# Performance work log

Hardware: AMD Instinct MI355X
Metric: run time of the kernel (lower is better)

## Reference

```python
import jax, jax.numpy as jnp
import numpy as np

B = 16384
SEQ_DIM = 512
EPI_DIM = 512
IN_DIM = SEQ_DIM + EPI_DIM   # 1024
OUT_DIM = 1024
N_EXPERTS = 8
LN_EPS = 1e-5


def setup_inputs() -> dict:
    key = jax.random.key(0)
    ks = jax.random.split(key, 10)
    s_in = 1.0 / np.sqrt(IN_DIM)
    s_out = 1.0 / np.sqrt(OUT_DIM)
    return {
        "z_s": jax.random.normal(ks[0], (B, SEQ_DIM), dtype=jnp.float32),
        "z_e": jax.random.normal(ks[1], (B, EPI_DIM), dtype=jnp.float32),
        # router: Linear(IN_DIM, N_EXPERTS)
        "router_w": jax.random.uniform(ks[2], (IN_DIM, N_EXPERTS), jnp.float32, -s_in, s_in),
        "router_b": jax.random.uniform(ks[3], (N_EXPERTS,), jnp.float32, -s_in, s_in),
        # expert layer 1: Linear(IN_DIM, OUT_DIM), stacked over experts
        "w1": jax.random.uniform(ks[4], (N_EXPERTS, IN_DIM, OUT_DIM), jnp.float32, -s_in, s_in),
        "b1": jax.random.uniform(ks[5], (N_EXPERTS, OUT_DIM), jnp.float32, -s_in, s_in),
        # expert layer 2: Linear(OUT_DIM, OUT_DIM)
        "w2": jax.random.uniform(ks[6], (N_EXPERTS, OUT_DIM, OUT_DIM), jnp.float32, -s_out, s_out),
        "b2": jax.random.uniform(ks[7], (N_EXPERTS, OUT_DIM), jnp.float32, -s_out, s_out),
        # per-expert LayerNorm affine params
        "gamma": jnp.ones((N_EXPERTS, OUT_DIM), dtype=jnp.float32),
        "beta": jnp.zeros((N_EXPERTS, OUT_DIM), dtype=jnp.float32),
    }


def reference(z_s, z_e, router_w, router_b, w1, b1, w2, b2, gamma, beta):
    combined = jnp.concatenate([z_s, z_e], axis=-1)            # [B, IN_DIM]
    weights = jax.nn.softmax(combined @ router_w + router_b, axis=-1)  # [B, E]
    # all experts as one batched GEMM (dropout = identity in eval mode)
    h = jnp.einsum('bi,eih->beh', combined, w1) + b1           # [B, E, H]
    h = jax.nn.gelu(h, approximate=False)
    y = jnp.einsum('beh,eho->beo', h, w2) + b2                 # [B, E, H]
    # per-expert LayerNorm over last dim
    mu = jnp.mean(y, axis=-1, keepdims=True)
    var = jnp.mean(jnp.square(y - mu), axis=-1, keepdims=True)
    y = (y - mu) * jax.lax.rsqrt(var + LN_EPS) * gamma + beta
    # softmax-weighted sum over experts
    z = jnp.einsum('be,beo->bo', weights, y)                   # [B, H]
    return z
```

## Files before the change

### kernel.cpp

```cpp
#include <hip/hip_runtime.h>
#include <cstdint>
#include <cstddef>

#define NEXP 8

typedef __attribute__((ext_vector_type(8))) short short8;
typedef __attribute__((ext_vector_type(4))) float f32x4;

static __device__ __forceinline__ float bf2f(unsigned short u) {
  union { unsigned int i; float f; } v; v.i = ((unsigned int)u) << 16; return v.f;
}
static __device__ __forceinline__ unsigned short f2bf(float f) {
  union { float f; unsigned int i; } v; v.f = f;
  unsigned int x = v.i;
  return (unsigned short)((x + 0x7fffu + ((x >> 16) & 1u)) >> 16);
}

static __device__ __forceinline__ float gelu_fast(float x) {
  const float u = 0.7978845608028654f * (x + 0.044715f * x * x * x);
  const float t = 1.0f - 2.0f / (__expf(2.0f * u) + 1.0f);
  return 0.5f * x * (1.0f + t);
}

__device__ __forceinline__ void gload16(const void* g, void* l) {
  __builtin_amdgcn_global_load_lds(
      (const __attribute__((address_space(1))) void*)g,
      (__attribute__((address_space(3))) void*)l, 16, 0, 0);
}

#define BAR() __builtin_amdgcn_s_barrier()
#define WAIT_LGKM0() asm volatile("s_waitcnt lgkmcnt(0)" ::: "memory")

__global__ __launch_bounds__(256) void prep_kernel(
    const float* __restrict__ z_s, const float* __restrict__ z_e,
    const float* __restrict__ rw, const float* __restrict__ rb,
    const float* __restrict__ w1, const float* __restrict__ w2,
    unsigned short* __restrict__ Xb, float* __restrict__ wts,
    unsigned short* __restrict__ wt1, unsigned short* __restrict__ wt2)
{
  __shared__ float red[4][NEXP];
  __shared__ unsigned short tile[32][33];
  const int bid = blockIdx.x;
  const int t = threadIdx.x;

  if (bid < 16384) {
    const int b = bid;
    const float* src = (t < 128) ? (z_s + (size_t)b * 512 + t * 4)
                                 : (z_e + (size_t)b * 512 + (t - 128) * 4);
    float4 v = *(const float4*)src;

    ushort4 o;
    o.x = f2bf(v.x); o.y = f2bf(v.y); o.z = f2bf(v.z); o.w = f2bf(v.w);
    *(ushort4*)(Xb + (size_t)b * 1024 + t * 4) = o;

    float acc[NEXP];
#pragma unroll
    for (int e = 0; e < NEXP; ++e) acc[e] = 0.f;

    const int k0 = t * 4;
    const float xv[4] = { v.x, v.y, v.z, v.w };
#pragma unroll
    for (int j = 0; j < 4; ++j) {
      const float x = xv[j];
      const float4* rwp = (const float4*)(rw + (size_t)(k0 + j) * NEXP);
      float4 r0 = rwp[0], r1 = rwp[1];
      acc[0] += x * r0.x; acc[1] += x * r0.y; acc[2] += x * r0.z; acc[3] += x * r0.w;
      acc[4] += x * r1.x; acc[5] += x * r1.y; acc[6] += x * r1.z; acc[7] += x * r1.w;
    }

#pragma unroll
    for (int off = 32; off; off >>= 1) {
#pragma unroll
      for (int e = 0; e < NEXP; ++e) acc[e] += __shfl_xor(acc[e], off);
    }
    if ((t & 63) == 0) {
#pragma unroll
      for (int e = 0; e < NEXP; ++e) red[t >> 6][e] = acc[e];
    }
    __syncthreads();
    if (t == 0) {
      float lg[NEXP];
      float mx = -1e30f;
#pragma unroll
      for (int e = 0; e < NEXP; ++e) {
        lg[e] = red[0][e] + red[1][e] + red[2][e] + red[3][e] + rb[e];
        mx = fmaxf(mx, lg[e]);
      }
      float sum = 0.f;
#pragma unroll
      for (int e = 0; e < NEXP; ++e) { lg[e] = expf(lg[e] - mx); sum += lg[e]; }
      const float inv = 1.f / sum;
#pragma unroll
      for (int e = 0; e < NEXP; ++e) wts[(size_t)b * NEXP + e] = lg[e] * inv;
    }
  } else {
    const int z = (bid - 16384) >> 10;
    const int r = (bid - 16384) & 1023;
    const int k0 = (r >> 5) * 32, n0 = (r & 31) * 32;
    const float* w = (z < 8) ? w1 : w2;
    unsigned short* wt = (z < 8) ? wt1 : wt2;
    const int e = z & 7;
    const int tx = t & 31, ty = t >> 5;

    const float* wp = w + ((size_t)e << 20) + (size_t)k0 * 1024 + n0;
#pragma unroll
    for (int i = 0; i < 4; ++i) {
      const int kk = ty + i * 8;
      tile[kk][tx] = f2bf(wp[(size_t)kk * 1024 + tx]);
    }
    __syncthreads();
    unsigned short* op = wt + ((size_t)e << 20) + (size_t)n0 * 1024 + k0;
#pragma unroll
    for (int i = 0; i < 4; ++i) {
      const int nn = ty + i * 8;
      op[(size_t)nn * 1024 + tx] = tile[tx][nn];
    }
  }
}

template <bool GELU>
__global__ __launch_bounds__(512, 2) void gemm8_kernel(
    const unsigned short* __restrict__ A,
    const unsigned short* __restrict__ Bt,
    const float* __restrict__ bias,
    unsigned short* __restrict__ C,
    long long strideAe, long long strideCe, int mtiles)
{
  __shared__ unsigned short lds[65536];

  const int nwg = gridDim.x;
  const int cpx = nwg >> 3;
  const int bid = blockIdx.x;
  const int swz = (bid & 7) * cpx + (bid >> 3);
  const int e   = swz / (mtiles << 2);
  const int rem = swz - e * (mtiles << 2);
  const int m0  = (rem >> 2) << 8;
  const int n0  = (rem & 3) << 8;

  const int t   = threadIdx.x;
  const int l   = t & 63;
  const int wid = t >> 6;
  const int wm  = wid >> 2;
  const int wn  = wid & 3;

  const unsigned short* Ae = A + (size_t)e * strideAe + (size_t)m0 * 1024;
  const unsigned short* Be = Bt + ((size_t)e << 20) + (size_t)n0 * 1024;

  const int sr = t >> 3;
  const int ss = ((t & 7) ^ ((t >> 3) & 7)) * 8;

  auto stageA = [&](int d, int h, int T) {
    const unsigned short* g = Ae + (size_t)(h * 128 + sr) * 1024 + T * 64 + ss;
    unsigned short* lp = lds + d * 32768 + h * 8192 + t * 8;
    gload16(g, lp);
    gload16(g + 65536, lp + 4096);
  };
  auto stageB = [&](int d, int h, int T) {
    const unsigned short* g = Be + (size_t)(h * 128 + sr) * 1024 + T * 64 + ss;
    unsigned short* lp = lds + 16384 + d * 32768 + h * 8192 + t * 8;
    gload16(g, lp);
    gload16(g + 65536, lp + 4096);
  };

  const int kq  = (l >> 4) ^ (l & 3);
  const int b2p = (l >> 2) & 1;
  const int sl0 = ((b2p << 2) | kq) * 8;
  const int sl1 = (((b2p ^ 1) << 2) | kq) * 8;
  const int aR = wm * 8192 + (l & 15) * 64;
  const int bR = 16384 + (wn >> 1) * 8192 + (wn & 1) * 4096 + (l & 15) * 64;

  short8 a[4][2], b0[2][2], b1[2][2];
  f32x4 acc[8][4];
#pragma unroll
  for (int i = 0; i < 8; ++i)
#pragma unroll
    for (int j = 0; j < 4; ++j) acc[i][j] = (f32x4){0.f, 0.f, 0.f, 0.f};

  auto ldA = [&](int d, int q) {
#pragma unroll
    for (int m = 0; m < 4; ++m) {
      const unsigned short* p = lds + d * 32768 + aR + (q * 4 + m) * 1024;
      a[m][0] = *(const short8*)(p + sl0);
      a[m][1] = *(const short8*)(p + sl1);
    }
  };
  auto ldB = [&](int d, int q, short8 (&br)[2][2]) {
#pragma unroll
    for (int n = 0; n < 2; ++n) {
      const unsigned short* p = lds + d * 32768 + bR + (q * 2 + n) * 1024;
      br[n][0] = *(const short8*)(p + sl0);
      br[n][1] = *(const short8*)(p + sl1);
    }
  };
  auto mmac = [&](int aq, int bq, short8 (&br)[2][2]) {
    __builtin_amdgcn_s_setprio(1);
#pragma unroll
    for (int ks = 0; ks < 2; ++ks)
#pragma unroll
      for (int m = 0; m < 4; ++m)
#pragma unroll
        for (int n = 0; n < 2; ++n)
          acc[aq * 4 + m][bq * 2 + n] = __builtin_amdgcn_mfma_f32_16x16x32_bf16(
              a[m][ks], br[n][ks], acc[aq * 4 + m][bq * 2 + n], 0, 0, 0);
    __builtin_amdgcn_s_setprio(0);
  };

  stageA(0, 0, 0); stageA(0, 1, 0); stageB(0, 0, 0); stageB(0, 1, 0);
  stageB(1, 0, 1); stageB(1, 1, 1); stageA(1, 0, 1);
  asm volatile("s_waitcnt vmcnt(6)" ::: "memory");
  BAR();

#pragma unroll 1
  for (int i = 0; i < 8; ++i) {
    const bool nl = (i < 7);
    const int T1 = 2 * i + 1, T2 = 2 * i + 2, T3 = 2 * i + 3;
    ldA(0, 0); ldB(0, 0, b0); stageA(1, 1, T1);
    asm volatile("s_waitcnt lgkmcnt(8)" ::: "memory");
    BAR(); WAIT_LGKM0();
    mmac(0, 0, b0);
    BAR();
    ldB(0, 1, b1);
    BAR(); WAIT_LGKM0();
    mmac(0, 1, b1);
    BAR();
    ldA(0, 1);
    if (nl) stageB(0, 0, T2);
    BAR(); WAIT_LGKM0();
    mmac(1, 1, b1);
    BAR();
    if (nl) { stageB(0, 1, T2); stageA(0, 0, T2); }
    BAR();
    mmac(1, 0, b0);
    if (nl) asm volatile("s_waitcnt vmcnt(6)" ::: "memory");
    else    asm volatile("s_waitcnt vmcnt(0)" ::: "memory");
    BAR();
    ldA(1, 0); ldB(1, 0, b0);
    if (nl) stageA(0, 1, T2);
    asm volatile("s_waitcnt lgkmcnt(8)" ::: "memory");
    BAR(); WAIT_LGKM0();
    mmac(0, 0, b0);
    BAR();
    ldB(1, 1, b1);
    BAR(); WAIT_LGKM0();
    mmac(0, 1, b1);
    BAR();
    ldA(1, 1);
    if (nl) stageB(1, 0, T3);
    BAR(); WAIT_LGKM0();
    mmac(1, 1, b1);
    BAR();
    if (nl) { stageB(1, 1, T3); stageA(1, 0, T3); }
    BAR();
    mmac(1, 0, b0);
    if (nl) asm volatile("s_waitcnt vmcnt(6)" ::: "memory");
    BAR();
  }

  const float* bp = bias + (size_t)e * 1024 + n0 + wn * 64;
  unsigned short* Ce = C + (size_t)e * strideCe + (size_t)(m0 + wm * 128) * 1024 + n0 + wn * 64;
  const int cr = (l >> 4) * 4, cc = l & 15;
#pragma unroll
  for (int mi = 0; mi < 8; ++mi) {
#pragma unroll
    for (int ni = 0; ni < 4; ++ni) {
      const int col = ni * 16 + cc;
      const float bv = bp[col];
#pragma unroll
      for (int r = 0; r < 4; ++r) {
        float v = acc[mi][ni][r] + bv;
        if (GELU) v = gelu_fast(v);
        Ce[(size_t)(mi * 16 + cr + r) * 1024 + col] = f2bf(v);
      }
    }
  }
}

__global__ __launch_bounds__(512) void finalize_kernel(
    const unsigned short* __restrict__ y,
    const float* __restrict__ wts,
    const float* __restrict__ gamma,
    const float* __restrict__ beta,
    float* __restrict__ zout,
    int Bc, int bbase)
{
  __shared__ float zacc[NEXP][1024];
  const int brow = blockIdx.x;
  const int t = threadIdx.x;
  const int e = t >> 6;
  const int lane = t & 63;

  const unsigned short* yp = y + ((size_t)e * Bc + brow) * 1024;
  short8 v0 = *(const short8*)(yp + lane * 8);
  short8 v1 = *(const short8*)(yp + 512 + lane * 8);

  float f0[8], f1[8];
  float s = 0.f, sq = 0.f;
#pragma unroll
  for (int j = 0; j < 8; ++j) {
    f0[j] = bf2f((unsigned short)v0[j]);
    f1[j] = bf2f((unsigned short)v1[j]);
    s += f0[j] + f1[j];
    sq += f0[j] * f0[j] + f1[j] * f1[j];
  }
#pragma unroll
  for (int off = 32; off; off >>= 1) {
    s  += __shfl_xor(s, off);
    sq += __shfl_xor(sq, off);
  }
  const float mu  = s * (1.f / 1024.f);
  const float var = sq * (1.f / 1024.f) - mu * mu;
  const float rs  = rsqrtf(var + 1e-5f);
  const float w   = wts[(size_t)(bbase + brow) * NEXP + e];

  const int c0 = lane * 8;
#pragma unroll
  for (int j = 0; j < 8; ++j) {
    const int ca = c0 + j, cb = 512 + c0 + j;
    zacc[e][ca] = w * ((f0[j] - mu) * rs * gamma[e * 1024 + ca] + beta[e * 1024 + ca]);
    zacc[e][cb] = w * ((f1[j] - mu) * rs * gamma[e * 1024 + cb] + beta[e * 1024 + cb]);
  }
  __syncthreads();
  float r0 = 0.f, r1 = 0.f;
#pragma unroll
  for (int ee = 0; ee < NEXP; ++ee) { r0 += zacc[ee][t]; r1 += zacc[ee][t + 512]; }
  float* zp = zout + (size_t)(bbase + brow) * 1024;
  zp[t] = r0;
  zp[t + 512] = r1;
}

extern "C" void kernel_launch(void* const* d_in, const int* in_sizes, int n_in,
                              void* d_out, int out_size, void* d_ws, size_t ws_size,
                              hipStream_t stream)
{
  const float* z_s      = (const float*)d_in[0];
  const float* z_e      = (const float*)d_in[1];
  const float* router_w = (const float*)d_in[2];
  const float* router_b = (const float*)d_in[3];
  const float* w1       = (const float*)d_in[4];
  const float* b1       = (const float*)d_in[5];
  const float* w2       = (const float*)d_in[6];
  const float* b2       = (const float*)d_in[7];
  const float* gamma    = (const float*)d_in[8];
  const float* beta     = (const float*)d_in[9];
  float* zout = (float*)d_out;

  const int B = 16384;

  char* ws = (char*)d_ws;
  unsigned short* Xb  = (unsigned short*)ws;
  unsigned short* W1t = (unsigned short*)(ws + 33554432);
  unsigned short* W2t = W1t + ((size_t)8 << 20);
  float* wts = (float*)(ws + 33554432 + 2 * 16777216);
  const size_t persist = 33554432 + 2 * 16777216 + 524288;
  char* dyn = ws + persist;
  const size_t rem = (ws_size > persist) ? (ws_size - persist) : 0;

  int nch = 2;
  while ((size_t)(B / nch) * 32768ull > rem && nch < 64) nch <<= 1;
  const int Bc = B / nch;

  unsigned short* hbuf = (unsigned short*)dyn;
  unsigned short* ybuf = hbuf + (size_t)Bc * 8 * 1024;

  prep_kernel<<<32768, 256, 0, stream>>>(z_s, z_e, router_w, router_b, w1, w2,
                                         Xb, wts, W1t, W2t);

  const int mt = Bc >> 8;
  const int nwg = mt * 32;

  for (int c = 0; c < nch; ++c) {
    const int bbase = c * Bc;
    gemm8_kernel<true><<<nwg, 512, 0, stream>>>(
        Xb + (size_t)bbase * 1024, W1t, b1, hbuf, 0ll, (long long)Bc * 1024, mt);
    gemm8_kernel<false><<<nwg, 512, 0, stream>>>(
        hbuf, W2t, b2, ybuf, (long long)Bc * 1024, (long long)Bc * 1024, mt);
    finalize_kernel<<<Bc, 512, 0, stream>>>(ybuf, wts, gamma, beta, zout, Bc, bbase);
  }
}
```

Before: 762.0 us.

## Fuse prep, both GEMMs and finalize into one persistent kernel with grid barriers

Replaces the prep kernel and the per-chunk GEMM1/GEMM2/finalize launches with a single persistent kernel of 256 workgroups. Phases are separated by atomic-counter grid barriers, and GEMM tiles and finalize rows are statically assigned per workgroup. The aim is to remove launch gaps and per-kernel tail effects between the many dependent stages. In exchange it adds spin-barrier overhead, relies on all 256 workgroups being co-resident to avoid deadlock, and runs the conversion/transpose prep with far fewer workgroups than before.

```diff
diff --git a/kernel.cpp b/kernel.cpp
--- a/kernel.cpp
+++ b/kernel.cpp
@@ -3,6 +3,7 @@
 #include <cstddef>
 
 #define NEXP 8
+#define NBLK 256
 
 typedef __attribute__((ext_vector_type(8))) short short8;
 typedef __attribute__((ext_vector_type(4))) float f32x4;
@@ -23,7 +24,8 @@
 }
 
 __device__ __forceinline__ void gload16(const void* g, void* l) {
-  __builtin_amdgcn_global_load_lds(
+  __builtin_amdgcn_global_lo\
+ad_lds(
       (const __attribute__((address_space(1))) void*)g,
       (__attribute__((address_space(3))) void*)l, 16, 0, 0);
 }
@@ -31,136 +33,36 @@
 #define BAR() __builtin_amdgcn_s_barrier()
 #define WAIT_LGKM0() asm volatile("s_waitcnt lgkmcnt(0)" ::: "memory")
 
-__global__ __launch_bounds__(256) void prep_kernel(
-    const float* __restrict__ z_s, const float* __restrict__ z_e,
-    const float* __restrict__ rw, const float* __restrict__ rb,
-    const float* __restrict__ w1, const float* __restrict__ w2,
-    unsigned short* __restrict__ Xb, float* __restrict__ wts,
-    unsigned short* __restrict__ wt1, unsigned short* __restrict__ wt2)
-{
-  __shared__ float red[4][NEXP];
-  __shared__ unsigned short tile[32][33];
-  const int bid = blockIdx.x;
-  const int t = threadIdx.x;
-
-  if (bid < 16384) {
-    const int b = bid;
-    const float* src = (t < 128) ? (z_s + (size_t)b * 512 + t * 4)
-                                 : (z_e + (size_t)b * 512 + (t - 128) * 4);
-    float4 v = *(const float4*)src;
-
-    ushort4 o;
-    o.x = f2bf(v.x); o.y = f2bf(v.y); o.z = f2bf(v.z); o.w = f2bf(v.w);
-    *(ushort4*)(Xb + (size_t)b * 1024 + t * 4) = o;
-
-    float acc[NEXP];
-#pragma unroll
-    for (int e = 0; e < NEXP; ++e) acc[e] = 0.f;
-
-    const int k0 = t * 4;
-    const float xv[4] = { v.x, v.y, v.z, v.w };
-#pragma unroll
-    for (int j = 0; j < 4; ++j) {
-      const float x = xv[j];
-      const float4* rwp = (const float4*)(rw + (size_t)(k0 + j) * NEXP);
-      float4 r0 = rwp[0], r1 = rwp[1];
-      acc[0] += x * r0.x; acc[1] += x * r0.y; acc[2] += x * r0.z; acc[3] += x * r0.w;
-      acc[4] += x * r1.x; acc[5] += x * r1.y; acc[6] += x * r1.z; acc[7] += x * r1.w;
-    }
-
-#pragma unroll
-    for (int off = 32; off; off >>= 1) {
-#pragma unroll
-      for (int e = 0; e < NEXP; ++e) acc[e] += __shfl_xor(acc[e], off);
-    }
-    if ((t & 63) == 0) {
-#pragma unroll
-      for (int e = 0; e < NEXP; ++e) red[t >> 6][e] = acc[e];
-    }
-    __syncthreads();
-    if (t == 0) {
-      float lg[NEXP];
-      float mx = -1e30f;
-#pragma unroll
-      for (int e = 0; e < NEXP; ++e) {
-        lg[e] = red[0][e] + red[1][e] + red[2][e] + red[3][e] + rb[e];
-        mx = fmaxf(mx, lg[e]);
-      }
-      float sum = 0.f;
-#pragma unroll
-      for (int e = 0; e < NEXP; ++e) { lg[e] = expf(lg[e] - mx); sum += lg[e]; }
-      const float inv = 1.f / sum;
-#pragma unroll
-      for (int e = 0; e < NEXP; ++e) wts[(size_t)b * NEXP + e] = lg[e] * inv;
-    }
-  } else {
-    const int z = (bid - 16384) >> 10;
-    const int r = (bid - 16384) & 1023;
-    const int k0 = (r >> 5) * 32, n0 = (r & 31) * 32;
-    const float* w = (z < 8) ? w1 : w2;
-    unsigned short* wt = (z < 8) ? wt1 : wt2;
-    const int e = z & 7;
-    const int tx = t & 31, ty = t >> 5;
-
-    const float* wp = w + ((size_t)e << 20) + (size_t)k0 * 1024 + n0;
-#pragma unroll
-    for (int i = 0; i < 4; ++i) {
-      const int kk = ty + i * 8;
-      tile[kk][tx] = f2bf(wp[(size_t)kk * 1024 + tx]);
-    }
-    __syncthreads();
-    unsigned short* op = wt + ((size_t)e << 20) + (size_t)n0 * 1024 + k0;
-#pragma unroll
-    for (int i = 0; i < 4; ++i) {
-      const int nn = ty + i * 8;
-      op[(size_t)nn * 1024 + tx] = tile[tx][nn];
-    }
-  }
+__device__ __forceinline__ void gridbar(int* bar, int idx) {
+  __syncthreads();
+  if (threadIdx.x == 0) {
+    __threadfence();
+    atomicAdd(&bar[idx], 1);
+    while (atomicAdd(&bar[idx], 0) < NBLK) __builtin_amdgcn_s_sleep(8);
+    __threadfence();
+  }
+  __syncthreads();
 }
 
 template <bool GELU>
-__global__ __launch_bounds__(512, 2) void gemm8_kernel(
+__device__ void gemm_phase(
+    unsigned short* lds,
     const unsigned short* __restrict__ A,
     const unsigned short* __restrict__ Bt,
     const float* __restrict__ bias,
     unsigned short* __restrict__ C,
-    long long strideAe, long long strideCe, int mtiles)
+    long long strideAe, long long strideCe,
+    int mt, int bid, int t)
 {
-  __shared__ unsigned short lds[65536];
-
-  const int nwg = gridDim.x;
-  const int cpx = nwg >> 3;
-  const int bid = blockIdx.x;
-  const int swz = (bid & 7) * cpx + (bid >> 3);
-  const int e   = swz / (mtiles << 2);
-  const int rem = swz - e * (mtiles << 2);
-  const int m0  = (rem >> 2) << 8;
-  const int n0  = (rem & 3) << 8;
-
-  const int t   = threadIdx.x;
+  const int e   = bid & 7;
+  const int sub = bid >> 3;
   const int l   = t & 63;
   const int wid = t >> 6;
   const int wm  = wid >> 2;
   const int wn  = wid & 3;
 
-  const unsigned short* Ae = A + (size_t)e * strideAe + (size_t)m0 * 1024;
-  const unsigned short* Be = Bt + ((size_t)e << 20) + (size_t)n0 * 1024;
-
   const int sr = t >> 3;
   const int ss = ((t & 7) ^ ((t >> 3) & 7)) * 8;
-
-  auto stageA = [&](int d, int h, int T) {
-    const unsigned short* g = Ae + (size_t)(h * 128 + sr) * 1024 + T * 64 + ss;
-    unsigned short* lp = lds + d * 32768 + h * 8192 + t * 8;
-    gload16(g, lp);
-    gload16(g + 65536, lp + 4096);
-  };
-  auto stageB = [&](int d, int h, int T) {
-    const unsigned short* g = Be + (size_t)(h * 128 + sr) * 1024 + T * 64 + ss;
-    unsigned short* lp = lds + 16384 + d * 32768 + h * 8192 + t * 8;
-    gload16(g, lp);
-    gload16(g + 65536, lp + 4096);
-  };
 
   const int kq  = (l >> 4) ^ (l & 3);
   const int b2p = (l >> 2) & 1;
@@ -169,163 +71,305 @@
   const int aR = wm * 8192 + (l & 15) * 64;
   const int bR = 16384 + (wn >> 1) * 8192 + (wn & 1) * 4096 + (l & 15) * 64;
 
-  short8 a[4][2], b0[2][2], b1[2][2];
-  f32x4 acc[8][4];
-#pragma unroll
-  for (int i = 0; i < 8; ++i)
-#pragma unroll
-    for (int j = 0; j < 4; ++j) acc[i][j] = (f32x4){0.f, 0.f, 0.f, 0.f};
-
-  auto ldA = [&](int d, int q) {
-#pragma unroll
-    for (int m = 0; m < 4; ++m) {
-      const unsigned short* p = lds + d * 32768 + aR + (q * 4 + m) * 1024;
-      a[m][0] = *(const short8*)(p + sl0);
-      a[m][1] = *(const short8*)(p + sl1);
-    }
-  };
-  auto ldB = [&](int d, int q, short8 (&br)[2][2]) {
-#pragma unroll
-    for (int n = 0; n < 2; ++n) {
-      const unsigned short* p = lds + d * 32768 + bR + (q * 2 + n) * 1024;
-      br[n][0] = *(const short8*)(p + sl0);
-      br[n][1] = *(const short8*)(p + sl1);
-    }
-  };
-  auto mmac = [&](int aq, int bq, short8 (&br)[2][2]) {
-    __builtin_amdgcn_s_setprio(1);
-#pragma unroll
-    for (int ks = 0; ks < 2; ++ks)
-#pragma unroll
-      for (int m = 0; m < 4; ++m)
-#pragma unroll
-        for (int n = 0; n < 2; ++n)
-          acc[aq * 4 + m][bq * 2 + n] = __builtin_amdgcn_mfma_f32_16x16x32_bf16(
-              a[m][ks], br[n][ks], acc[aq * 4 + m][bq * 2 + n], 0, 0, 0);
-    __builtin_amdgcn_s_setprio(0);
-  };
-
-  stageA(0, 0, 0); stageA(0, 1, 0); stageB(0, 0, 0); stageB(0, 1, 0);
-  stageB(1, 0, 1); stageB(1, 1, 1); stageA(1, 0, 1);
-  asm volatile("s_waitcnt vmcnt(6)" ::: "memory");
-  BAR();
-
-#pragma unroll 1
-  for (int i = 0; i < 8; ++i) {
-    const bool nl = (i < 7);
-    const int T1 = 2 * i + 1, T2 = 2 * i + 2, T3 = 2 * i + 3;
-    ldA(0, 0); ldB(0, 0, b0); stageA(1, 1, T1);
-    asm volatile("s_waitcnt lgkmcnt(8)" ::: "memory");
-    BAR(); WAIT_LGKM0();
-    mmac(0, 0, b0);
+  const int ntile = mt >> 3;
+#pragma unroll 1
+  for (int r = 0; r < ntile; ++r) {
+    const int tau = r * 32 + sub;
+    const int m0  = (tau % mt) << 8;
+    const int n0  = (tau / mt) << 8;
+
+    const unsigned short* Ae = A + (size_t)e * strideAe + (size_t)m0 * 1024;
+    const unsigned short* Be = Bt + ((size_t)e << 20) + (size_t)n0 * 1024;
+
+    auto stageA = [&](int d, int h, int T) {
+      const unsigned short* g = Ae + (size_t)(h * 128 + sr) * 1024 + T * 64 + ss;
+      unsigned short* lp = lds + d * 32768 + h * 8192 + t * 8;
+      gload16(g, lp);
+      gload16(g + 65536, lp + 4096);
+    };
+    auto stageB = [&](int d, int h, int T) {
+      const unsigned short* g = Be + (size_t)(h * 128 + sr) * 1024 + T * 64 + ss;
+      unsigned short* lp = lds + 16384 + d * 32768 + h * 8192 + t * 8;
+      gload16(g, lp);
+      gload16(g + 65536, lp + 4096);
+    };
+
+    short8 a[4][2], b0[2][2], b1[2][2];
+    f32x4 acc[8][4];
+#pragma unroll
+    for (int i = 0; i < 8; ++i)
+#pragma unroll
+      for (int j = 0; j < 4; ++j) acc[i][j] = (f32x4){0.f, 0.f, 0.f, 0.f};
+
+    auto ldA = [&](int d, int q) {
+#pragma unroll
+      for (int m = 0; m < 4; ++m) {
+        const unsigned short* p = lds + d * 32768 + aR + (q * 4 + m) * 1024;
+        a[m][0] = *(const short8*)(p + sl0);
+        a[m][1] = *(const short8*)(p + sl1);
+      }
+    };
+    auto ldB = [&](int d, int q, short8 (&br)[2][2]) {
+#pragma unroll
+      for (int n = 0; n < 2; ++n) {
+        const unsigned short* p = lds + d * 32768 + bR + (q * 2 + n) * 1024;
+        br[n][0] = *(const short8*)(p + sl0);
+        br[n][1] = *(const short8*)(p + sl1);
+      }
+    };
+    auto mmac = [&](int aq, int bq, short8 (&br)[2][2]) {
+      __builtin_amdgcn_s_setprio(1);
+#pragma unroll
+      for (int ks = 0; ks < 2; ++ks)
+#pragma unroll
+        for (int m = 0; m < 4; ++m)
+#pragma unroll
+          for (int n = 0; n < 2; ++n)
+            acc[aq * 4 + m][bq * 2 + n] = __builtin_amdgcn_mfma_f32_16x16x32_bf16(
+                a[m][ks], br[n][ks], acc[aq * 4 + m][bq * 2 + n], 0, 0, 0);
+      __builtin_amdgcn_s_setprio(0);
+    };
+
+    stageA(0, 0, 0); stageA(0, 1, 0); stageB(0, 0, 0); stageB(0, 1, 0);
+    stageB(1, 0, 1); stageB(1, 1, 1); stageA(1, 0, 1);
+    asm volatile("s_waitcnt vmcnt(6)" ::: "memory");
     BAR();
-    ldB(0, 1, b1);
-    BAR(); WAIT_LGKM0();
-    mmac(0, 1, b1);
-    BAR();
-    ldA(0, 1);
-    if (nl) stageB(0, 0, T2);
-    BAR(); WAIT_LGKM0();
-    mmac(1, 1, b1);
-    BAR();
-    if (nl) { stageB(0, 1, T2); stageA(0, 0, T2); }
-    BAR();
-    mmac(1, 0, b0);
-    if (nl) asm volatile("s_waitcnt vmcnt(6)" ::: "memory");
-    else    asm volatile("s_waitcnt vmcnt(0)" ::: "memory");
-    BAR();
-    ldA(1, 0); ldB(1, 0, b0);
-    if (nl) stageA(0, 1, T2);
-    asm volatile("s_waitcnt lgkmcnt(8)" ::: "memory");
-    BAR(); WAIT_LGKM0();
-    mmac(0, 0, b0);
-    BAR();
-    ldB(1, 1, b1);
-    BAR(); WAIT_LGKM0();
-    mmac(0, 1, b1);
-    BAR();
-    ldA(1, 1);
-    if (nl) stageB(1, 0, T3);
-    BAR(); WAIT_LGKM0();
-    mmac(1, 1, b1);
-    BAR();
-    if (nl) { stageB(1, 1, T3); stageA(1, 0, T3); }
-    BAR();
-    mmac(1, 0, b0);
-    if (nl) asm volatile("s_waitcnt vmcnt(6)" ::: "memory");
-    BAR();
-  }
-
-  const float* bp = bias + (size_t)e * 1024 + n0 + wn * 64;
-  unsigned short* Ce = C + (size_t)e * strideCe + (size_t)(m0 + wm * 128) * 1024 + n0 + wn * 64;
-  const int cr = (l >> 4) * 4, cc = l & 15;
-#pragma unroll
-  for (int mi = 0; mi < 8; ++mi) {
-#pragma unroll
-    for (int ni = 0; ni < 4; ++ni) {
-      const int col = ni * 16 + cc;
-      const float bv = bp[col];
-#pragma unroll
-      for (int r = 0; r < 4; ++r) {
-        float v = acc[mi][ni][r] + bv;
-        if (GELU) v = gelu_fast(v);
-        Ce[(size_t)(mi * 16 + cr + r) * 1024 + col] = f2bf(v);
-      }
-    }
-  }
-}
-
-__global__ __launch_bounds__(512) void finalize_kernel(
-    const unsigned short* __restrict__ y,
-    const float* __restrict__ wts,
-    const float* __restrict__ gamma,
-    const float* __restrict__ beta,
-    float* __restrict__ zout,
-    int Bc, int bbase)
+
+#pragma unroll 1
+    for (int i = 0; i < 8; ++i) {
+      const bool nl = (i < 7);
+      const int T1 = 2 * i + 1, T2 = 2 * i + 2, T3 = 2 * i + 3;
+      ldA(0, 0); ldB(0, 0, b0); stageA(1, 1, T1);
+      asm volatile("s_waitcnt lgkmcnt(8)" ::: "memory");
+      BAR(); WAIT_LGKM0();
+      mmac(0, 0, b0);
+      BAR();
+      ldB(0, 1, b1);
+      BAR(); WAIT_LGKM0();
+      mmac(0, 1, b1);
+      BAR();
+      ldA(0, 1);
+      if (nl) stageB(0, 0, T2);
+      BAR(); WAIT_LGKM0();
+      mmac(1, 1, b1);
+      BAR();
+      if (nl) { stageB(0, 1, T2); stageA(0, 0, T2); }
+      BAR();
+      mmac(1, 0, b0);
+      if (nl) asm volatile("s_waitcnt vmcnt(6)" ::: "memory");
+      else    asm volatile("s_waitcnt vmcnt(0)" ::: "memory");
+      BAR();
+      ldA(1, 0); ldB(1, 0, b0);
+      if (nl) stageA(0, 1, T2);
+      asm volatile("s_waitcnt lgkmcnt(8)" ::: "memory");
+      BAR(); WAIT_LGKM0();
+      mmac(0, 0, b0);
+      BAR();
+      ldB(1, 1, b1);
+      BAR(); WAIT_LGKM0();
+      mmac(0, 1, b1);
+      BAR();
+      ldA(1, 1);
+      if (nl) stageB(1, 0, T3);
+      BAR(); WAIT_LGKM0();
+      mmac(1, 1, b1);
+      BAR();
+      if (nl) { stageB(1, 1, T3); stageA(1, 0, T3); }
+      BAR();
+      mmac(1, 0, b0);
+      if (nl) asm volatile("s_waitcnt vmcnt(6)" ::: "memory");
+      BAR();
+    }
+
+    const float* bp = bias + (size_t)e * 1024 + n0 + wn * 64;
+    unsigned short* Ce = C + (size_t)e * strideCe + (size_t)(m0 + wm * 128) * 1024 + n0 + wn * 64;
+    const int cr = (l >> 4) * 4, cc = l & 15;
+#pragma unroll
+    for (int mi = 0; mi < 8; ++mi) {
+#pragma unroll
+      for (int ni = 0; ni < 4; ++ni) {
+        const int col = ni * 16 + cc;
+        const float bv = bp[col];
+#pragma unroll
+        for (int rr = 0; rr < 4; ++rr) {
+          float v = acc[mi][ni][rr] + bv;
+          if (GELU) v = gelu_fast(v);
+          Ce[(size_t)(mi * 16 + cr + rr) * 1024 + col] = f2bf(v);
+        }
+      }
+    }
+  }
+}
+
+__device__ void finalize_phase(
+    char* smem, const unsigned short* __restrict__ y, const float* __restrict__ wts,
+    const float* __restrict__ gamma, const float* __restrict__ beta,
+    float* __restrict__ zout, int Bc, int bbase, int bid, int t)
 {
-  __shared__ float zacc[NEXP][1024];
-  const int brow = blockIdx.x;
-  const int t = threadIdx.x;
+  float (*zacc)[1024] = (float(*)[1024])smem;
   const int e = t >> 6;
   const int lane = t & 63;
-
-  const unsigned short* yp = y + ((size_t)e * Bc + brow) * 1024;
-  short8 v0 = *(const short8*)(yp + lane * 8);
-  short8 v1 = *(const short8*)(yp + 512 + lane * 8);
-
-  float f0[8], f1[8];
-  float s = 0.f, sq = 0.f;
-#pragma unroll
-  for (int j = 0; j < 8; ++j) {
-    f0[j] = bf2f((unsigned short)v0[j]);
-    f1[j] = bf2f((unsigned short)v1[j]);
-    s += f0[j] + f1[j];
-    sq += f0[j] * f0[j] + f1[j] * f1[j];
-  }
-#pragma unroll
-  for (int off = 32; off; off >>= 1) {
-    s  += __shfl_xor(s, off);
-    sq += __shfl_xor(sq, off);
-  }
-  const float mu  = s * (1.f / 1024.f);
-  const float var = sq * (1.f / 1024.f) - mu * mu;
-  const float rs  = rsqrtf(var + 1e-5f);
-  const float w   = wts[(size_t)(bbase + brow) * NEXP + e];
-
-  const int c0 = lane * 8;
-#pragma unroll
-  for (int j = 0; j < 8; ++j) {
-    const int ca = c0 + j, cb = 512 + c0 + j;
-    zacc[e][ca] = w * ((f0[j] - mu) * rs * gamma[e * 1024 + ca] + beta[e * 1024 + ca]);
-    zacc[e][cb] = w * ((f1[j] - mu) * rs * gamma[e * 1024 + cb] + beta[e * 1024 + cb]);
-  }
-  __syncthreads();
-  float r0 = 0.f, r1 = 0.f;
-#pragma unroll
-  for (int ee = 0; ee < NEXP; ++ee) { r0 += zacc[ee][t]; r1 += zacc[ee][t + 512]; }
-  float* zp = zout + (size_t)(bbase + brow) * 1024;
-  zp[t] = r0;
-  zp[t + 512] = r1;
+  const int rows = Bc >> 8;
+#pragma unroll 1
+  for (int i = 0; i < rows; ++i) {
+    const int brow = bid * rows + i;
+    __syncthreads();
+
+    const unsigned short* yp = y + ((size_t)e * Bc + brow) * 1024;
+    short8 v0 = *(const short8*)(yp + lane * 8);
+    short8 v1 = *(const short8*)(yp + 512 + lane * 8);
+
+    float f0[8], f1[8];
+    float s = 0.f, sq = 0.f;
+#pragma unroll
+    for (int j = 0; j < 8; ++j) {
+      f0[j] = bf2f((unsigned short)v0[j]);
+      f1[j] = bf2f((unsigned short)v1[j]);
+      s += f0[j] + f1[j];
+      sq += f0[j] * f0[j] + f1[j] * f1[j];
+    }
+#pragma unroll
+    for (int off = 32; off; off >>= 1) {
+      s  += __shfl_xor(s, off);
+      sq += __shfl_xor(sq, off);
+    }
+    const float mu  = s * (1.f / 1024.f);
+    const float var = sq * (1.f / 1024.f) - mu * mu;
+    const float rs  = rsqrtf(var + 1e-5f);
+    const float w   = wts[(size_t)(bbase + brow) * NEXP + e];
+
+    const int c0 = lane * 8;
+#pragma unroll
+    for (int j = 0; j < 8; ++j) {
+      const int ca = c0 + j, cb = 512 + c0 + j;
+      zacc[e][ca] = w * ((f0[j] - mu) * rs * gamma[e * 1024 + ca] + beta[e * 1024 + ca]);
+      zacc[e][cb] = w * ((f1[j] - mu) * rs * gamma[e * 1024 + cb] + beta[e * 1024 + cb]);
+    }
+    __syncthreads();
+    float r0 = 0.f, r1 = 0.f;
+#pragma unroll
+    for (int ee = 0; ee < NEXP; ++ee) { r0 += zacc[ee][t]; r1 += zacc[ee][t + 512]; }
+    float* zp = zout + (size_t)(bbase + brow) * 1024;
+    zp[t] = r0;
+    zp[t + 512] = r1;
+  }
+}
+
+__global__ __launch_bounds__(512, 2) void moe_kernel(
+    const float* __restrict__ z_s, const float* __restrict__ z_e,
+    const float* __restrict__ rw, const float* __restrict__ rb,
+    const float* __restrict__ w1, const float* __restrict__ b1,
+    const float* __restrict__ w2, const float* __restrict__ b2,
+    const float* __restrict__ gamma, const float* __restrict__ beta,
+    unsigned short* __restrict__ Xb, float* __restrict__ wts,
+    unsigned short* __restrict__ W1t, unsigned short* __restrict__ W2t,
+    unsigned short* __restrict__ hbuf, unsigned short* __restrict__ ybuf,
+    float* __restrict__ zout, int* bar, int nch, int Bc)
+{
+  __shared__ __align__(16) char smem[131072];
+  unsigned short* lds = (unsigned short*)smem;
+  const int bid = blockIdx.x;
+  const int t = threadIdx.x;
+  const int mt = Bc >> 8;
+
+  {
+    const int wv = t >> 6, l = t & 63;
+#pragma unroll 1
+    for (int i = 0; i < 8; ++i) {
+      const int row = bid * 64 + i * 8 + wv;
+      const int k0 = l * 16;
+      const float* zp = (l < 32) ? (z_s + (size_t)row * 512 + k0)
+                                 : (z_e + (size_t)row * 512 + (k0 - 512));
+      const float4* zp4 = (const float4*)zp;
+      float4 va = zp4[0], vb = zp4[1], vc = zp4[2], vd = zp4[3];
+      const float x[16] = { va.x, va.y, va.z, va.w, vb.x, vb.y, vb.z, vb.w,
+                            vc.x, vc.y, vc.z, vc.w, vd.x, vd.y, vd.z, vd.w };
+      short8 s0, s1;
+#pragma unroll
+      for (int j = 0; j < 8; ++j) {
+        s0[j] = (short)f2bf(x[j]);
+        s1[j] = (short)f2bf(x[j + 8]);
+      }
+      *(short8*)(Xb + (size_t)row * 1024 + k0) = s0;
+      *(short8*)(Xb + (size_t)row * 1024 + k0 + 8) = s1;
+
+      float acc[NEXP];
+#pragma unroll
+      for (int e2 = 0; e2 < NEXP; ++e2) acc[e2] = 0.f;
+#pragma unroll
+      for (int j = 0; j < 16; ++j) {
+        const float4* rp = (const float4*)(rw + (size_t)(k0 + j) * NEXP);
+        float4 r0 = rp[0], r1 = rp[1];
+        acc[0] += x[j] * r0.x; acc[1] += x[j] * r0.y;
+        acc[2] += x[j] * r0.z; acc[3] += x[j] * r0.w;
+        acc[4] += x[j] * r1.x; acc[5] += x[j] * r1.y;
+        acc[6] += x[j] * r1.z; acc[7] += x[j] * r1.w;
+      }
+#pragma unroll
+      for (int off = 32; off; off >>= 1) {
+#pragma unroll
+        for (int e2 = 0; e2 < NEXP; ++e2) acc[e2] += __shfl_xor(acc[e2], off);
+      }
+      if (l < NEXP) {
+        float lg[NEXP];
+        float mx = -1e30f;
+#pragma unroll
+        for (int e2 = 0; e2 < NEXP; ++e2) {
+          lg[e2] = acc[e2] + rb[e2];
+          mx = fmaxf(mx, lg[e2]);
+        }
+        float sum = 0.f;
+#pragma unroll
+        for (int e2 = 0; e2 < NEXP; ++e2) sum += expf(lg[e2] - mx);
+        wts[(size_t)row * NEXP + l] = expf(lg[l] - mx) / sum;
+      }
+    }
+  }
+
+  {
+    unsigned short (*tile)[33] = (unsigned short(*)[33])(smem + (t >> 8) * (32 * 33 * 2));
+    const int tt = t & 255;
+    const int tx = tt & 31, ty = tt >> 5;
+#pragma unroll 1
+    for (int it = 0; it < 32; ++it) {
+      const int idx = bid * 64 + it * 2 + (t >> 8);
+      const int z = idx >> 10, r = idx & 1023;
+      const int k0 = (r >> 5) * 32, n0 = (r & 31) * 32;
+      const float* w = (z < 8) ? w1 : w2;
+      unsigned short* wt = (z < 8) ? W1t : W2t;
+      const int e = z & 7;
+      __syncthreads();
+      const float* wp = w + ((size_t)e << 20) + (size_t)k0 * 1024 + n0;
+#pragma unroll
+      for (int i = 0; i < 4; ++i) {
+        const int kk = ty + i * 8;
+        tile[kk][tx] = f2bf(wp[(size_t)kk * 1024 + tx]);
+      }
+      __syncthreads();
+      unsigned short* op = wt + ((size_t)e << 20) + (size_t)n0 * 1024 + k0;
+#pragma unroll
+      for (int i = 0; i < 4; ++i) {
+        const int nn = ty + i * 8;
+        op[(size_t)nn * 1024 + tx] = tile[tx][nn];
+      }
+    }
+  }
+
+  int bp = 0;
+  gridbar(bar, bp++);
+
+#pragma unroll 1
+  for (int c = 0; c < nch; ++c) {
+    const int bbase = c * Bc;
+    gemm_phase<true>(lds, Xb + (size_t)bbase * 1024, W1t, b1, hbuf,
+                     0ll, (long long)Bc * 1024, mt, bid, t);
+    gridbar(bar, bp++);
+    gemm_phase<false>(lds, hbuf, W2t, b2, ybuf,
+                      (long long)Bc * 1024, (long long)Bc * 1024, mt, bid, t);
+    gridbar(bar, bp++);
+    finalize_phase(smem, ybuf, wts, gamma, beta, zout, Bc, bbase, bid, t);
+    if (c + 1 < nch) gridbar(bar, bp++);
+  }
 }
 
 extern "C" void kernel_launch(void* const* d_in, const int* in_sizes, int n_in,
@@ -351,29 +395,21 @@
   unsigned short* W1t = (unsigned short*)(ws + 33554432);
   unsigned short* W2t = W1t + ((size_t)8 << 20);
   float* wts = (float*)(ws + 33554432 + 2 * 16777216);
-  const size_t persist = 33554432 + 2 * 16777216 + 524288;
+  int* bar   = (int*)(ws + 33554432 + 2 * 16777216 + 524288);
+  const size_t persist = 33554432 + 2 * 16777216 + 524288 + 256;
   char* dyn = ws + persist;
   const size_t rem = (ws_size > persist) ? (ws_size - persist) : 0;
 
   int nch = 2;
-  while ((size_t)(B / nch) * 32768ull > rem && nch < 64) nch <<= 1;
+  while ((size_t)(B / nch) * 32768ull > rem && nch < 8) nch <<= 1;
   const int Bc = B / nch;
 
   unsigned short* hbuf = (unsigned short*)dyn;
   unsigned short* ybuf = hbuf + (size_t)Bc * 8 * 1024;
 
-  prep_kernel<<<32768, 256, 0, stream>>>(z_s, z_e, router_w, router_b, w1, w2,
-                                         Xb, wts, W1t, W2t);
-
-  const int mt = Bc >> 8;
-  const int nwg = mt * 32;
-
-  for (int c = 0; c < nch; ++c) {
-    const int bbase = c * Bc;
-    gemm8_kernel<true><<<nwg, 512, 0, stream>>>(
-        Xb + (size_t)bbase * 1024, W1t, b1, hbuf, 0ll, (long long)Bc * 1024, mt);
-    gemm8_kernel<false><<<nwg, 512, 0, stream>>>(
-        hbuf, W2t, b2, ybuf, (long long)Bc * 1024, (long long)Bc * 1024, mt);
-    finalize_kernel<<<Bc, 512, 0, stream>>>(ybuf, wts, gamma, beta, zout, Bc, bbase);
-  }
-}
+  hipMemsetAsync(bar, 0, 256, stream);
+
+  moe_kernel<<<NBLK, 512, 0, stream>>>(
+      z_s, z_e, router_w, router_b, w1, b1, w2, b2, gamma, beta,
+      Xb, wts, W1t, W2t, hbuf, ybuf, zout, bar, nch, Bc);
+}
```

New measurement: 1.907 ms. +150.3%, slower.

## Have each GEMM workgroup compute two N tiles, prefetching the second during the epilogue

Applied to the files above, without the earlier changes.

Each gemm8 workgroup now computes two adjacent 256-wide N tiles of the same expert and M block in sequence, so the grid is halved. The prologue global-to-LDS loads for the second tile are issued before the first tile's bias/GELU/store epilogue, so that epilogue can overlap with the next tile's loads. This is meant to hide epilogue and prologue latency and reduce launch and tail effects. The cost is half as many workgroups for parallelism and a longer serial critical path per workgroup.

```diff
diff --git a/kernel.cpp b/kernel.cpp
--- a/kernel.cpp
+++ b/kernel.cpp
@@ -132,10 +132,11 @@
   const int cpx = nwg >> 3;
   const int bid = blockIdx.x;
   const int swz = (bid & 7) * cpx + (bid >> 3);
-  const int e   = swz / (mtiles << 2);
-  const int rem = swz - e * (mtiles << 2);
-  const int m0  = (rem >> 2) << 8;
-  const int n0  = (rem & 3) << 8;
+  const int ppe = mtiles << 1;
+  const int e   = swz / ppe;
+  const int rem = swz - e * ppe;
+  const int m0  = (rem >> 1) << 8;
+  const int np  = rem & 1;
 
   const int t   = threadIdx.x;
   const int l   = t & 63;
@@ -143,8 +144,9 @@
   const int wm  = wid >> 2;
   const int wn  = wid & 3;
 
-  const unsigned short* Ae = A + (size_t)e * strideAe + (size_t)m0 * 1024;
-  const unsigned short* Be = Bt + ((size_t)e << 20) + (size_t)n0 * 1024;
+  const unsigned short* Ae  = A + (size_t)e * strideAe + (size_t)m0 * 1024;
+  const unsigned short* Be0 = Bt + ((size_t)e << 20) + ((size_t)((np << 1) + 0) << 8) * 1024;
+  const unsigned short* Be1 = Bt + ((size_t)e << 20) + ((size_t)((np << 1) + 1) << 8) * 1024;
 
   const int sr = t >> 3;
   const int ss = ((t & 7) ^ ((t >> 3) & 7)) * 8;
@@ -155,11 +157,15 @@
     gload16(g, lp);
     gload16(g + 65536, lp + 4096);
   };
-  auto stageB = [&](int d, int h, int T) {
+  auto stageB = [&](const unsigned short* Be, int d, int h, int T) {
     const unsigned short* g = Be + (size_t)(h * 128 + sr) * 1024 + T * 64 + ss;
     unsigned short* lp = lds + 16384 + d * 32768 + h * 8192 + t * 8;
     gload16(g, lp);
     gload16(g + 65536, lp + 4096);
+  };
+  auto prologue = [&](const unsigned short* Be) {
+    stageA(0, 0, 0); stageA(0, 1, 0); stageB(Be, 0, 0, 0); stageB(Be, 0, 1, 0);
+    stageB(Be, 1, 0, 1); stageB(Be, 1, 1, 1); stageA(1, 0, 1);
   };
 
   const int kq  = (l >> 4) ^ (l & 3);
@@ -171,10 +177,6 @@
 
   short8 a[4][2], b0[2][2], b1[2][2];
   f32x4 acc[8][4];
-#pragma unroll
-  for (int i = 0; i < 8; ++i)
-#pragma unroll
-    for (int j = 0; j < 4; ++j) acc[i][j] = (f32x4){0.f, 0.f, 0.f, 0.f};
 
   auto ldA = [&](int d, int q) {
 #pragma unroll
@@ -205,72 +207,88 @@
     __builtin_amdgcn_s_setprio(0);
   };
 
-  stageA(0, 0, 0); stageA(0, 1, 0); stageB(0, 0, 0); stageB(0, 1, 0);
-  stageB(1, 0, 1); stageB(1, 1, 1); stageA(1, 0, 1);
+  prologue(Be0);
   asm volatile("s_waitcnt vmcnt(6)" ::: "memory");
   BAR();
 
 #pragma unroll 1
-  for (int i = 0; i < 8; ++i) {
-    const bool nl = (i < 7);
-    const int T1 = 2 * i + 1, T2 = 2 * i + 2, T3 = 2 * i + 3;
-    ldA(0, 0); ldB(0, 0, b0); stageA(1, 1, T1);
-    asm volatile("s_waitcnt lgkmcnt(8)" ::: "memory");
-    BAR(); WAIT_LGKM0();
-    mmac(0, 0, b0);
-    BAR();
-    ldB(0, 1, b1);
-    BAR(); WAIT_LGKM0();
-    mmac(0, 1, b1);
-    BAR();
-    ldA(0, 1);
-    if (nl) stageB(0, 0, T2);
-    BAR(); WAIT_LGKM0();
-    mmac(1, 1, b1);
-    BAR();
-    if (nl) { stageB(0, 1, T2); stageA(0, 0, T2); }
-    BAR();
-    mmac(1, 0, b0);
-    if (nl) asm volatile("s_waitcnt vmcnt(6)" ::: "memory");
-    else    asm volatile("s_waitcnt vmcnt(0)" ::: "memory");
-    BAR();
-    ldA(1, 0); ldB(1, 0, b0);
-    if (nl) stageA(0, 1, T2);
-    asm volatile("s_waitcnt lgkmcnt(8)" ::: "memory");
-    BAR(); WAIT_LGKM0();
-    mmac(0, 0, b0);
-    BAR();
-    ldB(1, 1, b1);
-    BAR(); WAIT_LGKM0();
-    mmac(0, 1, b1);
-    BAR();
-    ldA(1, 1);
-    if (nl) stageB(1, 0, T3);
-    BAR(); WAIT_LGKM0();
-    mmac(1, 1, b1);
-    BAR();
-    if (nl) { stageB(1, 1, T3); stageA(1, 0, T3); }
-    BAR();
-    mmac(1, 0, b0);
-    if (nl) asm volatile("s_waitcnt vmcnt(6)" ::: "memory");
-    BAR();
-  }
-
-  const float* bp = bias + (size_t)e * 1024 + n0 + wn * 64;
-  unsigned short* Ce = C + (size_t)e * strideCe + (size_t)(m0 + wm * 128) * 1024 + n0 + wn * 64;
-  const int cr = (l >> 4) * 4, cc = l & 15;
-#pragma unroll
-  for (int mi = 0; mi < 8; ++mi) {
-#pragma unroll
-    for (int ni = 0; ni < 4; ++ni) {
-      const int col = ni * 16 + cc;
-      const float bv = bp[col];
-#pragma unroll
-      for (int r = 0; r < 4; ++r) {
-        float v = acc[mi][ni][r] + bv;
-        if (GELU) v = gelu_fast(v);
-        Ce[(size_t)(mi * 16 + cr + r) * 1024 + col] = f2bf(v);
+  for (int tl = 0; tl < 2; ++tl) {
+    const unsigned short* Be = (tl == 0) ? Be0 : Be1;
+    const int n0 = ((np << 1) | tl) << 8;
+
+#pragma unroll
+    for (int i = 0; i < 8; ++i)
+#pragma unroll
+      for (int j = 0; j < 4; ++j) acc[i][j] = (f32x4){0.f, 0.f, 0.f, 0.f};
+
+#pragma unroll 1
+    for (int i = 0; i < 8; ++i) {
+      const bool nl = (i < 7);
+      const int T1 = 2 * i + 1, T2 = 2 * i + 2, T3 = 2 * i + 3;
+      ldA(0, 0); ldB(0, 0, b0); stageA(1, 1, T1);
+      asm volatile("s_waitcnt lgkmcnt(8)" ::: "memory");
+      BAR(); WAIT_LGKM0();
+      mmac(0, 0, b0);
+      BAR();
+      ldB(0, 1, b1);
+      BAR(); WAIT_LGKM0();
+      mmac(0, 1, b1);
+      BAR();
+      ldA(0, 1);
+      if (nl) stageB(Be, 0, 0, T2);
+      BAR(); WAIT_LGKM0();
+      mmac(1, 1, b1);
+      BAR();
+      if (nl) { stageB(Be, 0, 1, T2); stageA(0, 0, T2); }
+      BAR();
+      mmac(1, 0, b0);
+      if (nl) asm volatile("s_waitcnt vmcnt(6)" ::: "memory");
+      else    asm volatile("s_waitcnt vmcnt(0)" ::: "memory");
+      BAR();
+      ldA(1, 0); ldB(1, 0, b0);
+      if (nl) stageA(0, 1, T2);
+      asm volatile("s_waitcnt lgkmcnt(8)" ::: "memory");
+      BAR(); WAIT_LGKM0();
+      mmac(0, 0, b0);
+      BAR();
+      ldB(1, 1, b1);
+      BAR(); WAIT_LGKM0();
+      mmac(0, 1, b1);
+      BAR();
+      ldA(1, 1);
+      if (nl) stageB(Be, 1, 0, T3);
+      BAR(); WAIT_LGKM0();
+      mmac(1, 1, b1);
+      BAR();
+      if (nl) { stageB(Be, 1, 1, T3); stageA(1, 0, T3); }
+      BAR();
+      mmac(1, 0, b0);
+      if (nl) asm volatile("s_waitcnt vmcnt(6)" ::: "memory");
+      BAR();
+    }
+    if (tl == 0) prologue(Be1);
+
+    const float* bp = bias + (size_t)e * 1024 + n0 + wn * 64;
+    unsigned short* Ce = C + (size_t)e * strideCe + (size_t)(m0 + wm * 128) * 1024 + n0 + wn * 64;
+    const int cr = (l >> 4) * 4, cc = l & 15;
+#pragma unroll
+    for (int mi = 0; mi < 8; ++mi) {
+#pragma unroll
+      for (int ni = 0; ni < 4; ++ni) {
+        const int col = ni * 16 + cc;
+        const float bv = bp[col];
+#pragma unroll
+        for (int r = 0; r < 4; ++r) {
+          float v = acc[mi][ni][r] + bv;
+          if (GELU) v = gelu_fast(v);
+          Ce[(size_t)(mi * 16 + cr + r) * 1024 + col] = f2bf(v);
+        }
       }
+    }
+
+    if (tl == 0) {
+      asm volatile("s_waitcnt vmcnt(6)" ::: "memory");
+      BAR();
     }
   }
 }
@@ -366,7 +384,7 @@
                                          Xb, wts, W1t, W2t);
 
   const int mt = Bc >> 8;
-  const int nwg = mt * 32;
+  const int nwg = mt * 16;
 
   for (int c = 0; c < nch; ++c) {
     const int bbase = c * Bc;
```

New measurement: 1.842 ms. +141.8%, slower.
